# Optimization experiments

Measured on AMD Instinct MI355X. Metric: run time of the kernel, lower is better.

The kernel has to match this reference:

```python
import jax, jax.numpy as jnp
import numpy as np

B, S, D_IN = 2, 2048, 2048
H, KVH, HD = 32, 8, 64
GROUPS = H // KVH
EPS = 1e-6
SCALE = HD ** -0.5


def setup_inputs() -> dict:
    key = jax.random.key(0)
    ks = jax.random.split(key, 6)
    x = jax.random.normal(ks[0], (B, S, D_IN), jnp.float32)
    Wq = jax.random.normal(ks[1], (H * HD, D_IN), jnp.float32) * 0.02
    Wk = jax.random.normal(ks[2], (KVH * HD, D_IN), jnp.float32) * 0.02
    Wv = jax.random.normal(ks[3], (KVH * HD, D_IN), jnp.float32) * 0.02
    Wo = jax.random.normal(ks[4], (D_IN, H * HD), jnp.float32) * 0.02
    w_qnorm = jnp.ones((HD,), jnp.float32)
    w_knorm = jnp.ones((HD,), jnp.float32)
    # Llama-style RoPE tables: [S, HD] with frequencies duplicated across halves
    inv_freq = 1.0 / (10000.0 ** (np.arange(0, HD, 2, dtype=np.float32) / HD))
    ang = np.outer(np.arange(S, dtype=np.float32), inv_freq)  # [S, HD/2]
    emb = np.concatenate([ang, ang], axis=-1)  # [S, HD]
    cos = jnp.asarray(np.cos(emb), jnp.float32)
    sin = jnp.asarray(np.sin(emb), jnp.float32)
    mask = jnp.tril(jnp.ones((S, S), jnp.bool_))  # unused by module (causal hardcoded)
    return dict(x=x, mask=mask, cos=cos, sin=sin, Wq=Wq, Wk=Wk, Wv=Wv, Wo=Wo,
                w_qnorm=w_qnorm, w_knorm=w_knorm)


def _rms_norm(t, w):
    # per-head-dim RMSNorm, eps inside sqrt (torch nn.RMSNorm semantics)
    var = jnp.mean(jnp.square(t), axis=-1, keepdims=True)
    return t * jax.lax.rsqrt(var + EPS) * w


def _rotate_half(t):
    t1, t2 = jnp.split(t, 2, axis=-1)
    return jnp.concatenate([-t2, t1], axis=-1)


def _rope(t, cos, sin):
    # t: [B,H,S,HD]; cos/sin: [S,HD]
    return t * cos[None, None] + _rotate_half(t) * sin[None, None]


def reference(x, mask, cos, sin, Wq, Wk, Wv, Wo, w_qnorm, w_knorm):
    bs, seq, _ = x.shape
    q = (x @ Wq.T).reshape(bs, seq, H, HD).transpose(0, 2, 1, 3)    # [B,H,S,hd]
    k = (x @ Wk.T).reshape(bs, seq, KVH, HD).transpose(0, 2, 1, 3)  # [B,KVH,S,hd]
    v = (x @ Wv.T).reshape(bs, seq, KVH, HD).transpose(0, 2, 1, 3)
    # GQA: repeat_interleave KV over head dim
    k = jnp.repeat(k, GROUPS, axis=1)
    v = jnp.repeat(v, GROUPS, axis=1)
    # fused QK RMSNorm then RoPE
    q = _rope(_rms_norm(q, w_qnorm), cos, sin)
    k = _rope(_rms_norm(k, w_knorm), cos, sin)
    # causal attention
    scores = jnp.einsum('bhqd,bhkd->bhqk', q, k) * SCALE
    causal = jnp.arange(seq)[:, None] >= jnp.arange(seq)[None, :]
    scores = jnp.where(causal, scores, jnp.finfo(scores.dtype).min)
    attn = jax.nn.softmax(scores, axis=-1)
    out = jnp.einsum('bhqk,bhkd->bhqd', attn, v)
    out = out.transpose(0, 2, 1, 3).reshape(bs, seq, H * HD)
    return out @ Wo.T
```

## Files before the change

### kernel.cpp

```cpp
#include <hip/hip_runtime.h>

typedef __bf16 bf16_t;
typedef __bf16 bf16x8 __attribute__((ext_vector_type(8)));
typedef __bf16 bf16x4 __attribute__((ext_vector_type(4)));
typedef float f32x4 __attribute__((ext_vector_type(4)));
typedef unsigned int u32;

#define AS1 __attribute__((address_space(1)))
#define AS3 __attribute__((address_space(3)))

#define ASTR 72

#if __has_builtin(__builtin_amdgcn_exp2f)
#define EXP2(x) __builtin_amdgcn_exp2f(x)
#else
#define EXP2(x) exp2f(x)
#endif

__device__ __forceinline__ void g2l16(const bf16_t* g, bf16_t* l) {
  __builtin_amdgcn_global_load_lds((const AS1 u32*)g, (AS3 u32*)l, 16, 0, 0);
}

__device__ __forceinline__ u32 pkbf(float a, float b) {
  u32 ua = __builtin_bit_cast(u32, a) + 0x8000u;
  u32 ub = __builtin_bit_cast(u32, b) + 0x8000u;
  return (ua >> 16) | (ub & 0xFFFF0000u);
}

__global__ __launch_bounds__(256) void cvt5(
    const float* __restrict__ s0, const float* __restrict__ s1,
    const float* __restrict__ s2, const float* __restrict__ s3,
    const float* __restrict__ s4,
    bf16_t* __restrict__ d0, bf16_t* __restrict__ d1, bf16_t* __restrict__ d2,
    bf16_t* __restrict__ d3, bf16_t* __restrict__ d4)
{
  int blk = blockIdx.x;
  const float* s; bf16_t* d; int off;
  if      (blk <  8192) { s = s0; d = d0; off = blk;         }
  else if (blk < 12288) { s = s1; d = d1; off = blk -  8192; }
  else if (blk < 13312) { s = s2; d = d2; off = blk - 12288; }
  else if (blk < 14336) { s = s3; d = d3; off = blk - 13312; }
  else                  { s = s4; d = d4; off = blk - 14336; }
  size_t i = (size_t)off * 1024 + threadIdx.x * 4;
  float4 v = *(const float4*)&s[i];
  bf16x4 t;
  t[0] = (bf16_t)v.x; t[1] = (bf16_t)v.y; t[2] = (bf16_t)v.z; t[3] = (bf16_t)v.w;
  *(bf16x4*)&d[i] = t;
}

__device__ __forceinline__ void gemm_core(
    const bf16_t* __restrict__ A, const bf16_t* __restrict__ B, int K,
    bf16_t* As0, bf16_t* As1, bf16_t* Bs0, bf16_t* Bs1, f32x4 (&acc)[4][4])
{
  const int tid = threadIdx.x, lane = tid & 63, w = tid >> 6;
  const int col = lane & 15, quad = lane >> 4;
  const int wm = w >> 1, wn = w & 1;
  const int lr = lane >> 2;
  const int lc = (((lane & 3) ^ ((lane >> 3) & 3)) << 3);
  const int sw = ((quad ^ ((col >> 1) & 3)) << 3);
  const bf16_t* ga = A + (size_t)(w * 16 + lr) * K + lc;
  const bf16_t* gb = B + (size_t)(w * 16 + lr) * K + lc;
  const int lo0 = (w * 16) * 32, lo1 = (64 + w * 16) * 32;

  g2l16(ga,                  As0 + lo0);
  g2l16(ga + (size_t)64 * K, As0 + lo1);
  g2l16(gb,                  Bs0 + lo0);
  g2l16(gb + (size_t)64 * K, Bs0 + lo1);

  const int nkb = K >> 5;
  for (int kb = 0; kb < nkb; ++kb) {
    __syncthreads();
    bf16_t* Ac = (kb & 1) ? As1 : As0;
    bf16_t* Bc = (kb & 1) ? Bs1 : Bs0;
    if (kb + 1 < nkb) {
      bf16_t* An = (kb & 1) ? As0 : As1;
      bf16_t* Bn = (kb & 1) ? Bs0 : Bs1;
      const int k2 = (kb + 1) * 32;
      g2l16(ga + k2,                  An + lo0);
      g2l16(ga + k2 + (size_t)64 * K, An + lo1);
      g2l16(gb + k2,                  Bn + lo0);
      g2l16(gb + k2 + (size_t)64 * K, Bn + lo1);
    }

    bf16x8 af[4], bfr[4];
#pragma unroll
    for (int mt = 0; mt < 4; ++mt)
      af[mt] = *(const bf16x8*)&Ac[(wm * 64 + mt * 16 + col) * 32 + sw];
#pragma unroll
    for (int nt = 0; nt < 4; ++nt)
      bfr[nt] = *(const bf16x8*)&Bc[(wn * 64 + nt * 16 + col) * 32 + sw];
#pragma unroll
    for (int mt = 0; mt < 4; ++mt)
#pragma unroll
      for (int nt = 0; nt < 4; ++nt)
        acc[mt][nt] = __builtin_amdgcn_mfma_f32_16x16x32_bf16(af[mt], bfr[nt], acc[mt][nt], 0, 0, 0);
  }
}

__global__ __launch_bounds__(256, 4) void gemm_qkv(
    const bf16_t* __restrict__ xb, const bf16_t* __restrict__ Wqb,
    const bf16_t* __restrict__ Wkb, const bf16_t* __restrict__ Wvb,
    const float* __restrict__ cosT, const float* __restrict__ sinT,
    const float* __restrict__ wq, const float* __restrict__ wk,
    bf16_t* __restrict__ Qn, bf16_t* __restrict__ Kn, bf16_t* __restrict__ Vp)
{
  __shared__ bf16_t As[2][128 * 32], Bs[2][128 * 32];
  const int bn = blockIdx.x, bm = blockIdx.y;
  const bf16_t* B;
  if      (bn < 16) B = Wqb + (size_t)bn * 128 * 2048;
  else if (bn < 20) B = Wkb + (size_t)(bn - 16) * 128 * 2048;
  else              B = Wvb + (size_t)(bn - 20) * 128 * 2048;

  f32x4 acc[4][4] = {};
  gemm_core(xb + (size_t)bm * 128 * 2048, B, 2048, As[0], As[1], Bs[0], Bs[1], acc);

  const int lane = threadIdx.x & 63, w = threadIdx.x >> 6;
  const int col = lane & 15, quad = lane >> 4, wm = w >> 1, wn = w & 1;

  if (bn < 20) {
    const bool isQ = bn < 16;
    const float* wnv = isQ ? wq : wk;
    float w4[4];
#pragma unroll
    for (int nt = 0; nt < 4; ++nt) w4[nt] = wnv[nt * 16 + col];
    bf16_t* dst = isQ ? Qn + ((size_t)(bn * 2 + wn)) * 2048 * 64
                      : Kn + ((size_t)((bn - 16) * 2 + wn)) * 2048 * 64;
    const size_t bstride = isQ ? (size_t)32 * 2048 * 64 : (size_t)8 * 2048 * 64;
    const float qscale = 0.125f * 1.4426950408889634f;

#pragma unroll
    for (int mt = 0; mt < 4; ++mt)
#pragma unroll
      for (int r = 0; r < 4; ++r) {
        int row = bm * 128 + wm * 64 + mt * 16 + quad * 4 + r;
        int b = row >> 11, s = row & 2047;
        float v[4], ss = 0.f;
#pragma unroll
        for (int nt = 0; nt < 4; ++nt) { v[nt] = acc[mt][nt][r]; ss += v[nt] * v[nt]; }
        ss += __shfl_xor(ss, 1, 64);
        ss += __shfl_xor(ss, 2, 64);
        ss += __shfl_xor(ss, 4, 64);
        ss += __shfl_xor(ss, 8, 64);
        float rr = rsqrtf(ss * (1.0f / 64.0f) + 1e-6f);
        float t[4];
#pragma unroll
        for (int nt = 0; nt < 4; ++nt) t[nt] = v[nt] * rr * w4[nt];
        bf16_t* drow = dst + b * bstride + (size_t)s * 64;
#pragma unroll
        for (int nt = 0; nt < 4; ++nt) {
          int hd = nt * 16 + col;
          float rot = (nt < 2) ? -t[nt + 2] : t[nt - 2];
          float ov = t[nt] * cosT[s * 64 + hd] + rot * sinT[s * 64 + hd];
          if (isQ) ov *= qscale;
          drow[hd] = (bf16_t)ov;
        }
      }
  } else {
    const int cb = (bn - 20) * 128;
#pragma unroll
    for (int mt = 0; mt < 4; ++mt)
#pragma unroll
      for (int r = 0; r < 4; ++r) {
        int row = bm * 128 + wm * 64 + mt * 16 + quad * 4 + r;
        bf16_t* crow = Vp + (size_t)row * 512 + cb + wn * 64 + col;
#pragma unroll
        for (int nt = 0; nt < 4; ++nt)
          crow[nt * 16] = (bf16_t)acc[mt][nt][r];
      }
  }
}

__global__ __launch_bounds__(256, 4) void gemm_o(
    const bf16_t* __restrict__ Ao, const bf16_t* __restrict__ Wob,
    float* __restrict__ Cf)
{
  __shared__ bf16_t As[2][128 * 32], Bs[2][128 * 32];
  const int bn = blockIdx.x, bm = blockIdx.y;
  f32x4 acc[4][4] = {};
  gemm_core(Ao + (size_t)bm * 128 * 2048, Wob + (size_t)bn * 128 * 2048, 2048,
            As[0], As[1], Bs[0], Bs[1], acc);

  const int lane = threadIdx.x & 63, w = threadIdx.x >> 6;
  const int col = lane & 15, quad = lane >> 4, wm = w >> 1, wn = w & 1;
#pragma unroll
  for (int mt = 0; mt < 4; ++mt)
#pragma unroll
    for (int r = 0; r < 4; ++r) {
      int row = bm * 128 + wm * 64 + mt * 16 + quad * 4 + r;
      float* crow = Cf + (size_t)row * 2048 + bn * 128 + wn * 64 + col;
#pragma unroll
      for (int nt = 0; nt < 4; ++nt)
        crow[nt * 16] = acc[mt][nt][r];
    }
}

__global__ __launch_bounds__(256) void vtrans(
    const bf16_t* __restrict__ Vp, bf16_t* __restrict__ Vt)
{
  __shared__ bf16_t T[64 * 136];
  const int st = blockIdx.x, kvh = blockIdx.y, b = blockIdx.z;
  const int tid = threadIdx.x;
#pragma unroll
  for (int p = 0; p < 4; ++p) {
    int r = p * 32 + (tid >> 3);
    int c = (tid & 7) * 8;
    bf16x8 v = *(const bf16x8*)&Vp[((size_t)(b * 2048 + st * 128 + r)) * 512 + kvh * 64 + c];
#pragma unroll
    for (int i = 0; i < 8; ++i) T[(c + i) * 136 + r] = v[i];
  }
  __syncthreads();
#pragma unroll
  for (int p = 0; p < 4; ++p) {
    int hd = p * 16 + (tid >> 4);
    int sc = (tid & 15) * 8;
    bf16x8 v = *(const bf16x8*)&T[hd * 136 + sc];
    *(bf16x8*)&Vt[((size_t)((b * 8 + kvh) * 64) + hd) * 2048 + st * 128 + sc] = v;
  }
}

__global__ __launch_bounds__(256, 3) void attn(
    const bf16_t* __restrict__ Qn, const bf16_t* __restrict__ Kn,
    const bf16_t* __restrict__ Vt, bf16_t* __restrict__ Ao)
{
  __shared__ bf16_t KsL[2][64 * 32], KsH[2][64 * 32];
  __shared__ bf16_t VsL[2][64 * 32], VsH[2][64 * 32];
  __shared__ bf16_t Ps[128 * ASTR];

  const int tid = threadIdx.x, lane = tid & 63, w = tid >> 6;
  const int col = lane & 15, quad = lane >> 4;
  const int lr = lane >> 2;
  const int lcs = (((lane & 3) ^ ((lane >> 3) & 3)) << 3);
  const int sw  = ((quad ^ ((col >> 1) & 3)) << 3);
  const int h = blockIdx.x, b = blockIdx.y;
  const int qt = 15 - blockIdx.z;
  const int kvh = h >> 2;

  const bf16_t* Kb = Kn + ((size_t)(b * 8 + kvh)) * 2048 * 64;
  const bf16_t* Vb = Vt + ((size_t)(b * 8 + kvh)) * 64 * 2048;
  const bf16_t* Qb = Qn + (((size_t)(b * 32 + h)) * 2048 + qt * 128) * 64;
  const int lw = w * 512;

  bf16x8 Qf[2][2];
#pragma unroll
  for (int mt = 0; mt < 2; ++mt)
#pragma unroll
    for (int kk = 0; kk < 2; ++kk)
      Qf[mt][kk] = *(const bf16x8*)&Qb[(w * 32 + mt * 16 + col) * 64 + kk * 32 + quad * 8];

  bf16x8 ones;
#pragma unroll
  for (int i = 0; i < 8; ++i) ones[i] = (bf16_t)1.0f;

  f32x4 o[2][4] = {};
  f32x4 lacc[2] = {};

  const int rowmin = qt * 128 + w * 32;
  const int rowmax = rowmin + 31;
  const int jmax = 2 * qt + 1;

  {
    const bf16_t* gk = &Kb[(size_t)(w * 16 + lr) * 64 + lcs];
    const bf16_t* gv = &Vb[(size_t)(w * 16 + lr) * 2048 + lcs];
    g2l16(gk,      &KsL[0][lw]);
    g2l16(gk + 32, &KsH[0][lw]);
    g2l16(gv,      &VsL[0][lw]);
    g2l16(gv + 32, &VsH[0][lw]);
  }

  for (int j = 0; j <= jmax; ++j) {
    __syncthreads();
    if (j < jmax) {
      const int nb = (j + 1) & 1;
      const bf16_t* gk = &Kb[(size_t)((j + 1) * 64 + w * 16 + lr) * 64 + lcs];
      const bf16_t* gv = &Vb[(size_t)(w * 16 + lr) * 2048 + (j + 1) * 64 + lcs];
      g2l16(gk,      &KsL[nb][lw]);
      g2l16(gk + 32, &KsH[nb][lw]);
      g2l16(gv,      &VsL[nb][lw]);
      g2l16(gv + 32, &VsH[nb][lw]);
    }

    if (j * 64 <= rowmax) {
      const int bf = j & 1;
      const bool needmask = (j * 64 + 63 > rowmin);

#pragma unroll
      for (int kt = 0; kt < 4; ++kt) {
        bf16x8 kf0 = *(const bf16x8*)&KsL[bf][(kt * 16 + col) * 32 + sw];
        bf16x8 kf1 = *(const bf16x8*)&KsH[bf][(kt * 16 + col) * 32 + sw];
        f32x4 st0 = {}, st1 = {};
        st0 = __builtin_amdgcn_mfma_f32_16x16x32_bf16(kf0, Qf[0][0], st0, 0, 0, 0);
        st0 = __builtin_amdgcn_mfma_f32_16x16x32_bf16(kf1, Qf[0][1], st0, 0, 0, 0);
        st1 = __builtin_amdgcn_mfma_f32_16x16x32_bf16(kf0, Qf[1][0], st1, 0, 0, 0);
        st1 = __builtin_amdgcn_mfma_f32_16x16x32_bf16(kf1, Qf[1][1], st1, 0, 0, 0);
        const int k0 = j * 64 + kt * 16 + quad * 4;
#pragma unroll
        for (int mt = 0; mt < 2; ++mt) {
          f32x4 st = mt ? st1 : st0;
          float p0 = EXP2(st[0]), p1 = EXP2(st[1]);
          float p2 = EXP2(st[2]), p3 = EXP2(st[3]);
          if (needmask) {
            const int qg = qt * 128 + w * 32 + mt * 16 + col;
            p0 = (k0 + 0 > qg) ? 0.f : p0;
            p1 = (k0 + 1 > qg) ? 0.f : p1;
            p2 = (k0 + 2 > qg) ? 0.f : p2;
            p3 = (k0 + 3 > qg) ? 0.f : p3;
          }
          uint2 pk = { pkbf(p0, p1), pkbf(p2, p3) };
          *(uint2*)&Ps[(w * 32 + mt * 16 + col) * ASTR + kt * 16 + quad * 4] = pk;
        }
      }
      asm volatile("s_waitcnt lgkmcnt(0)" ::: "memory");

#pragma unroll
      for (int kk = 0; kk < 2; ++kk) {
        const bf16_t* Vh = kk ? &VsH[bf][0] : &VsL[bf][0];
        bf16x8 pa0 = *(const bf16x8*)&Ps[(w * 32 + col) * ASTR + kk * 32 + quad * 8];
        bf16x8 pa1 = *(const bf16x8*)&Ps[(w * 32 + 16 + col) * ASTR + kk * 32 + quad * 8];
        lacc[0] = __builtin_amdgcn_mfma_f32_16x16x32_bf16(pa0, ones, lacc[0], 0, 0, 0);
        lacc[1] = __builtin_amdgcn_mfma_f32_16x16x32_bf16(pa1, ones, lacc[1], 0, 0, 0);
#pragma unroll
        for (int nt = 0; nt < 4; ++nt) {
          bf16x8 vf = *(const bf16x8*)&Vh[(nt * 16 + col) * 32 + sw];
          o[0][nt] = __builtin_amdgcn_mfma_f32_16x16x32_bf16(pa0, vf, o[0][nt], 0, 0, 0);
          o[1][nt] = __builtin_amdgcn_mfma_f32_16x16x32_bf16(pa1, vf, o[1][nt], 0, 0, 0);
        }
      }
    }
  }

#pragma unroll
  for (int mt = 0; mt < 2; ++mt)
#pragma unroll
    for (int r = 0; r < 4; ++r) {
      float inv = 1.0f / lacc[mt][r];
      int row = b * 2048 + qt * 128 + w * 32 + mt * 16 + quad * 4 + r;
      bf16_t* orow = &Ao[(size_t)row * 2048 + h * 64 + col];
#pragma unroll
      for (int nt = 0; nt < 4; ++nt)
        orow[nt * 16] = (bf16_t)(o[mt][nt][r] * inv);
    }
}

extern "C" void kernel_launch(void* const* d_in, const int* in_sizes, int n_in,
                              void* d_out, int out_size, void* d_ws, size_t ws_size,
                              hipStream_t stream)
{
  const float* x    = (const float*)d_in[0];
  const float* cosT = (const float*)d_in[2];
  const float* sinT = (const float*)d_in[3];
  const float* Wq   = (const float*)d_in[4];
  const float* Wk   = (const float*)d_in[5];
  const float* Wv   = (const float*)d_in[6];
  const float* Wo   = (const float*)d_in[7];
  const float* wq   = (const float*)d_in[8];
  const float* wk   = (const float*)d_in[9];
  float* out = (float*)d_out;

  char* ws = (char*)d_ws;
  bf16_t* xb  = (bf16_t*)(ws);
  bf16_t* Ao  = (bf16_t*)(ws);
  bf16_t* Wqb = (bf16_t*)(ws + 16777216);
  bf16_t* Vt  = (bf16_t*)(ws + 16777216);
  bf16_t* Wkb = (bf16_t*)(ws + 25165824);
  bf16_t* Wvb = (bf16_t*)(ws + 27262976);
  bf16_t* Wob = (bf16_t*)(ws + 29360128);
  bf16_t* Vp  = (bf16_t*)(ws + 37748736);
  bf16_t* Qn  = (bf16_t*)(ws + 41943040);
  bf16_t* Kn  = (bf16_t*)(ws + 58720256);

  cvt5<<<18432, 256, 0, stream>>>(x, Wq, Wk, Wv, Wo, xb, Wqb, Wkb, Wvb, Wob);
  gemm_qkv<<<dim3(24, 32), 256, 0, stream>>>(xb, Wqb, Wkb, Wvb, cosT, sinT, wq, wk, Qn, Kn, Vp);
  vtrans<<<dim3(16, 8, 2), 256, 0, stream>>>(Vp, Vt);
  attn<<<dim3(32, 2, 16), 256, 0, stream>>>(Qn, Kn, Vt, Ao);
  gemm_o<<<dim3(16, 32), 256, 0, stream>>>(Ao, Wob, out);
}
```

Baseline: 298.6 us.

## Use 256x256 tiles with 4-stage pipelined 8-wave GEMM for QKV projection

Replaces the 128x128, 4-wave, double-buffered QKV GEMM with a 256x256, 8-wave kernel that keeps a 4-deep shared-memory ring fed by direct global-to-LDS loads. MFMA work is interleaved with prefetch, and the kernel raises wave priority around the MFMA blocks. Workgroup indices are remapped into an XCD-aware order to improve L2 reuse. The larger tiles are meant to raise arithmetic intensity and overlap loads with compute. In exchange the grid shrinks to 192 blocks, which may underfill 256 CUs, and the 128 KB of LDS per block limits occupancy.

After: 308.9 us. +3.5%, slower.

```diff
diff --git a/kernel.cpp b/kernel.cpp
--- a/kernel.cpp
+++ b/kernel.cpp
@@ -97,46 +97,121 @@
   }
 }
 
-__global__ __launch_bounds__(256, 4) void gemm_qkv(
+__device__ __forceinline__ void gemm_core8(
+    const bf16_t* __restrict__ A, const bf16_t* __restrict__ B,
+    bf16_t (&As)[4][8192], bf16_t (&Bs)[4][8192], f32x4 (&acc)[8][4])
+{
+  constexpr int NT = 64;
+  const int tid = threadIdx.x, lane = tid & 63, w = tid >> 6;
+  const int col = lane & 15, quad = lane >> 4;
+  const int wm = w >> 2, wn = w & 3;
+  const int lr = lane >> 2;
+  const int lc = (((lane & 3) ^ ((lane >> 3) & 3)) << 3);
+  const int sw = ((quad ^ ((col >> 1) & 3)) << 3);
+  const bf16_t* ga = A + (size_t)(w * 16 + lr) * 2048 + lc;
+  const bf16_t* gb = B + (size_t)(w * 16 + lr) * 2048 + lc;
+  const int lo0 = w * 512, lo1 = 4096 + w * 512;
+
+#pragma unroll
+  for (int tt = 0; tt < 3; ++tt) {
+    g2l16(ga + tt * 32,                      &As[tt][lo0]);
+    g2l16(ga + tt * 32 + (size_t)128 * 2048, &As[tt][lo1]);
+    g2l16(gb + tt * 32,                      &Bs[tt][lo0]);
+    g2l16(gb + tt * 32 + (size_t)128 * 2048, &Bs[tt][lo1]);
+  }
+  asm volatile("s_waitcnt vmcnt(8)" ::: "memory");
+  __builtin_amdgcn_s_barrier();
+
+  for (int t = 0; t < NT; ++t) {
+    const bf16_t* Ac = As[t & 3];
+    const bf16_t* Bc = Bs[t & 3];
+    const int pf = t + 3;
+    bf16x8 bfrg[4], afrg[4];
+
+#pragma unroll
+    for (int nf = 0; nf < 4; ++nf)
+      bfrg[nf] = *(const bf16x8*)&Bc[(wn * 64 + nf * 16 + col) * 32 + sw];
+#pragma unroll
+    for (int mf = 0; mf < 4; ++mf)
+      afrg[mf] = *(const bf16x8*)&Ac[(wm * 128 + mf * 16 + col) * 32 + sw];
+    if (pf < NT) {
+      g2l16(ga + pf * 32,                      &As[pf & 3][lo0]);
+      g2l16(ga + pf * 32 + (size_t)128 * 2048, &As[pf & 3][lo1]);
+    }
+    __builtin_amdgcn_s_barrier();
+    __builtin_amdgcn_s_setprio(1);
+#pragma unroll
+    for (int mf = 0; mf < 4; ++mf)
+#pragma unroll
+      for (int nf = 0; nf < 4; ++nf)
+        acc[mf][nf] = __builtin_amdgcn_mfma_f32_16x16x32_bf16(afrg[mf], bfrg[nf], acc[mf][nf], 0, 0, 0);
+    __builtin_amdgcn_s_setprio(0);
+    __builtin_amdgcn_s_barrier();
+
+#pragma unroll
+    for (int mf = 0; mf < 4; ++mf)
+      afrg[mf] = *(const bf16x8*)&Ac[(wm * 128 + (mf + 4) * 16 + col) * 32 + sw];
+    if (pf < NT) {
+      g2l16(gb + pf * 32,                      &Bs[pf & 3][lo0]);
+      g2l16(gb + pf * 32 + (size_t)128 * 2048, &Bs[pf & 3][lo1]);
+    }
+    __builtin_amdgcn_s_barrier();
+    __builtin_amdgcn_s_setprio(1);
+#pragma unroll
+    for (int mf = 0; mf < 4; ++mf)
+#pragma unroll
+      for (int nf = 0; nf < 4; ++nf)
+        acc[mf + 4][nf] = __builtin_amdgcn_mfma_f32_16x16x32_bf16(afrg[mf], bfrg[nf], acc[mf + 4][nf], 0, 0, 0);
+    __builtin_amdgcn_s_setprio(0);
+    if (t < NT - 3)       asm volatile("s_waitcnt vmcnt(8)" ::: "memory");
+    else if (t == NT - 3) asm volatile("s_waitcnt vmcnt(4)" ::: "memory");
+    else if (t == NT - 2) asm volatile("s_waitcnt vmcnt(0)" ::: "memory");
+    __builtin_amdgcn_s_barrier();
+  }
+}
+
+__global__ __launch_bounds__(512, 2) void gemm_qkv8(
     const bf16_t* __restrict__ xb, const bf16_t* __restrict__ Wqb,
     const bf16_t* __restrict__ Wkb, const bf16_t* __restrict__ Wvb,
     const float* __restrict__ cosT, const float* __restrict__ sinT,
     const float* __restrict__ wq, const float* __restrict__ wk,
     bf16_t* __restrict__ Qn, bf16_t* __restrict__ Kn, bf16_t* __restrict__ Vp)
 {
-  __shared__ bf16_t As[2][128 * 32], Bs[2][128 * 32];
-  const int bn = blockIdx.x, bm = blockIdx.y;
-  const bf16_t* B;
-  if      (bn < 16) B = Wqb + (size_t)bn * 128 * 2048;
-  else if (bn < 20) B = Wkb + (size_t)(bn - 16) * 128 * 2048;
-  else              B = Wvb + (size_t)(bn - 20) * 128 * 2048;
-
-  f32x4 acc[4][4] = {};
-  gemm_core(xb + (size_t)bm * 128 * 2048, B, 2048, As[0], As[1], Bs[0], Bs[1], acc);
+  __shared__ bf16_t As[4][8192], Bs[4][8192];
+  const int bid = blockIdx.x;
+  const int f = (bid & 7) * 24 + (bid >> 3);
+  const int bm = f / 12, bn = f % 12;
+  const bf16_t* Bp;
+  if      (bn <  8) Bp = Wqb + (size_t)bn * 256 * 2048;
+  else if (bn < 10) Bp = Wkb + (size_t)(bn - 8) * 256 * 2048;
+  else              Bp = Wvb + (size_t)(bn - 10) * 256 * 2048;
+
+  f32x4 acc[8][4] = {};
+  gemm_core8(xb + (size_t)bm * 256 * 2048, Bp, As, Bs, acc);
 
   const int lane = threadIdx.x & 63, w = threadIdx.x >> 6;
-  const int col = lane & 15, quad = lane >> 4, wm = w >> 1, wn = w & 1;
-
-  if (bn < 20) {
-    const bool isQ = bn < 16;
+  const int col = lane & 15, quad = lane >> 4, wm = w >> 2, wn = w & 3;
+
+  if (bn < 10) {
+    const bool isQ = bn < 8;
     const float* wnv = isQ ? wq : wk;
     float w4[4];
 #pragma unroll
-    for (int nt = 0; nt < 4; ++nt) w4[nt] = wnv[nt * 16 + col];
-    bf16_t* dst = isQ ? Qn + ((size_t)(bn * 2 + wn)) * 2048 * 64
-                      : Kn + ((size_t)((bn - 16) * 2 + wn)) * 2048 * 64;
+    for (int nf = 0; nf < 4; ++nf) w4[nf] = wnv[nf * 16 + col];
+    const int head = isQ ? bn * 4 + wn : (bn - 8) * 4 + wn;
+    bf16_t* dst = (isQ ? Qn : Kn) + (size_t)head * 2048 * 64;
     const size_t bstride = isQ ? (size_t)32 * 2048 * 64 : (size_t)8 * 2048 * 64;
     const float qscale = 0.125f * 1.4426950408889634f;
 
 #pragma unroll
-    for (int mt = 0; mt < 4; ++mt)
+    for (int mf = 0; mf < 8; ++mf)
 #pragma unroll
       for (int r = 0; r < 4; ++r) {
-        int row = bm * 128 + wm * 64 + mt * 16 + quad * 4 + r;
+        int row = bm * 256 + wm * 128 + mf * 16 + quad * 4 + r;
         int b = row >> 11, s = row & 2047;
         float v[4], ss = 0.f;
 #pragma unroll
-        for (int nt = 0; nt < 4; ++nt) { v[nt] = acc[mt][nt][r]; ss += v[nt] * v[nt]; }
+        for (int nf = 0; nf < 4; ++nf) { v[nf] = acc[mf][nf][r]; ss += v[nf] * v[nf]; }
         ss += __shfl_xor(ss, 1, 64);
         ss += __shfl_xor(ss, 2, 64);
         ss += __shfl_xor(ss, 4, 64);
@@ -144,28 +219,28 @@
         float rr = rsqrtf(ss * (1.0f / 64.0f) + 1e-6f);
         float t[4];
 #pragma unroll
-        for (int nt = 0; nt < 4; ++nt) t[nt] = v[nt] * rr * w4[nt];
+        for (int nf = 0; nf < 4; ++nf) t[nf] = v[nf] * rr * w4[nf];
         bf16_t* drow = dst + b * bstride + (size_t)s * 64;
 #pragma unroll
-        for (int nt = 0; nt < 4; ++nt) {
-          int hd = nt * 16 + col;
-          float rot = (nt < 2) ? -t[nt + 2] : t[nt - 2];
-          float ov = t[nt] * cosT[s * 64 + hd] + rot * sinT[s * 64 + hd];
+        for (int nf = 0; nf < 4; ++nf) {
+          int hd = nf * 16 + col;
+          float rot = (nf < 2) ? -t[nf + 2] : t[nf - 2];
+          float ov = t[nf] * cosT[s * 64 + hd] + rot * sinT[s * 64 + hd];
           if (isQ) ov *= qscale;
           drow[hd] = (bf16_t)ov;
         }
       }
   } else {
-    const int cb = (bn - 20) * 128;
-#pragma unroll
-    for (int mt = 0; mt < 4; ++mt)
+    const int cb = (bn - 10) * 256;
+#pragma unroll
+    for (int mf = 0; mf < 8; ++mf)
 #pragma unroll
       for (int r = 0; r < 4; ++r) {
-        int row = bm * 128 + wm * 64 + mt * 16 + quad * 4 + r;
+        int row = bm * 256 + wm * 128 + mf * 16 + quad * 4 + r;
         bf16_t* crow = Vp + (size_t)row * 512 + cb + wn * 64 + col;
 #pragma unroll
-        for (int nt = 0; nt < 4; ++nt)
-          crow[nt * 16] = (bf16_t)acc[mt][nt][r];
+        for (int nf = 0; nf < 4; ++nf)
+          crow[nf * 16] = (bf16_t)acc[mf][nf][r];
       }
   }
 }
@@ -369,7 +444,7 @@
   bf16_t* Kn  = (bf16_t*)(ws + 58720256);
 
   cvt5<<<18432, 256, 0, stream>>>(x, Wq, Wk, Wv, Wo, xb, Wqb, Wkb, Wvb, Wob);
-  gemm_qkv<<<dim3(24, 32), 256, 0, stream>>>(xb, Wqb, Wkb, Wvb, cosT, sinT, wq, wk, Qn, Kn, Vp);
+  gemm_qkv8<<<192, 512, 0, stream>>>(xb, Wqb, Wkb, Wvb, cosT, sinT, wq, wk, Qn, Kn, Vp);
   vtrans<<<dim3(16, 8, 2), 256, 0, stream>>>(Vp, Vt);
   attn<<<dim3(32, 2, 16), 256, 0, stream>>>(Qn, Kn, Vt, Ao);
   gemm_o<<<dim3(16, 32), 256, 0, stream>>>(Ao, Wob, out);
```

## Triple-buffer GEMM LDS tiles with vmcnt-based waits and single barrier

Applied to the files above, without the earlier changes.

Replaces the double-buffered GEMM mainloop used by the QKV and output projections with a three-stage LDS ring. Loads run two K-steps ahead, and explicit s_waitcnt vmcnt plus a raw s_barrier replace the top-of-loop __syncthreads. The aim is to hide more global-load latency behind the MFMA work. In exchange, LDS per block grows to 48KB, and launch bounds drop from 4 to 3 blocks per CU, which may reduce occupancy.

Result: slower. 314.3 us (+5.2%).

```diff
diff --git a/kernel.cpp b/kernel.cpp
--- a/kernel.cpp
+++ b/kernel.cpp
@@ -48,9 +48,9 @@
   *(bf16x4*)&d[i] = t;
 }
 
-__device__ __forceinline__ void gemm_core(
+__device__ __forceinline__ void gemm_core3(
     const bf16_t* __restrict__ A, const bf16_t* __restrict__ B, int K,
-    bf16_t* As0, bf16_t* As1, bf16_t* Bs0, bf16_t* Bs1, f32x4 (&acc)[4][4])
+    bf16_t (&As)[3][4096], bf16_t (&Bs)[3][4096], f32x4 (&acc)[4][4])
 {
   const int tid = threadIdx.x, lane = tid & 63, w = tid >> 6;
   const int col = lane & 15, quad = lane >> 4;
@@ -62,26 +62,28 @@
   const bf16_t* gb = B + (size_t)(w * 16 + lr) * K + lc;
   const int lo0 = (w * 16) * 32, lo1 = (64 + w * 16) * 32;
 
-  g2l16(ga,                  As0 + lo0);
-  g2l16(ga + (size_t)64 * K, As0 + lo1);
-  g2l16(gb,                  Bs0 + lo0);
-  g2l16(gb + (size_t)64 * K, Bs0 + lo1);
-
   const int nkb = K >> 5;
+
+  g2l16(ga,      &As[0][lo0]); g2l16(ga + (size_t)64 * K,      &As[0][lo1]);
+  g2l16(gb,      &Bs[0][lo0]); g2l16(gb + (size_t)64 * K,      &Bs[0][lo1]);
+  g2l16(ga + 32, &As[1][lo0]); g2l16(ga + 32 + (size_t)64 * K, &As[1][lo1]);
+  g2l16(gb + 32, &Bs[1][lo0]); g2l16(gb + 32 + (size_t)64 * K, &Bs[1][lo1]);
+  asm volatile("s_waitcnt vmcnt(4)" ::: "memory");
+  __builtin_amdgcn_s_barrier();
+
   for (int kb = 0; kb < nkb; ++kb) {
-    __syncthreads();
-    bf16_t* Ac = (kb & 1) ? As1 : As0;
-    bf16_t* Bc = (kb & 1) ? Bs1 : Bs0;
-    if (kb + 1 < nkb) {
-      bf16_t* An = (kb & 1) ? As0 : As1;
-      bf16_t* Bn = (kb & 1) ? Bs0 : Bs1;
-      const int k2 = (kb + 1) * 32;
-      g2l16(ga + k2,                  An + lo0);
-      g2l16(ga + k2 + (size_t)64 * K, An + lo1);
-      g2l16(gb + k2,                  Bn + lo0);
-      g2l16(gb + k2 + (size_t)64 * K, Bn + lo1);
-    }
-
+    if (kb + 2 < nkb) {
+      const int sl = (kb + 2) % 3;
+      const int k2 = (kb + 2) * 32;
+      g2l16(ga + k2,                  &As[sl][lo0]);
+      g2l16(ga + k2 + (size_t)64 * K, &As[sl][lo1]);
+      g2l16(gb + k2,                  &Bs[sl][lo0]);
+      g2l16(gb + k2 + (size_t)64 * K, &Bs[sl][lo1]);
+    }
+
+    const int cu = kb % 3;
+    const bf16_t* Ac = As[cu];
+    const bf16_t* Bc = Bs[cu];
     bf16x8 af[4], bfr[4];
 #pragma unroll
     for (int mt = 0; mt < 4; ++mt)
@@ -94,17 +96,25 @@
 #pragma unroll
       for (int nt = 0; nt < 4; ++nt)
         acc[mt][nt] = __builtin_amdgcn_mfma_f32_16x16x32_bf16(af[mt], bfr[nt], acc[mt][nt], 0, 0, 0);
-  }
-}
-
-__global__ __launch_bounds__(256, 4) void gemm_qkv(
+
+    if (kb + 2 < nkb) {
+      asm volatile("s_waitcnt vmcnt(4)" ::: "memory");
+      __builtin_amdgcn_s_barrier();
+    } else if (kb + 1 < nkb) {
+      asm volatile("s_waitcnt vmcnt(0)" ::: "memory");
+      __builtin_amdgcn_s_barrier();
+    }
+  }
+}
+
+__global__ __launch_bounds__(256, 3) void gemm_qkv(
     const bf16_t* __restrict__ xb, const bf16_t* __restrict__ Wqb,
     const bf16_t* __restrict__ Wkb, const bf16_t* __restrict__ Wvb,
     const float* __restrict__ cosT, const float* __restrict__ sinT,
     const float* __restrict__ wq, const float* __restrict__ wk,
     bf16_t* __restrict__ Qn, bf16_t* __restrict__ Kn, bf16_t* __restrict__ Vp)
 {
-  __shared__ bf16_t As[2][128 * 32], Bs[2][128 * 32];
+  __shared__ bf16_t As[3][4096], Bs[3][4096];
   const int bn = blockIdx.x, bm = blockIdx.y;
   const bf16_t* B;
   if      (bn < 16) B = Wqb + (size_t)bn * 128 * 2048;
@@ -112,7 +122,7 @@
   else              B = Wvb + (size_t)(bn - 20) * 128 * 2048;
 
   f32x4 acc[4][4] = {};
-  gemm_core(xb + (size_t)bm * 128 * 2048, B, 2048, As[0], As[1], Bs[0], Bs[1], acc);
+  gemm_core3(xb + (size_t)bm * 128 * 2048, B, 2048, As, Bs, acc);
 
   const int lane = threadIdx.x & 63, w = threadIdx.x >> 6;
   const int col = lane & 15, quad = lane >> 4, wm = w >> 1, wn = w & 1;
@@ -170,15 +180,15 @@
   }
 }
 
-__global__ __launch_bounds__(256, 4) void gemm_o(
+__global__ __launch_bounds__(256, 3) void gemm_o(
     const bf16_t* __restrict__ Ao, const bf16_t* __restrict__ Wob,
     float* __restrict__ Cf)
 {
-  __shared__ bf16_t As[2][128 * 32], Bs[2][128 * 32];
+  __shared__ bf16_t As[3][4096], Bs[3][4096];
   const int bn = blockIdx.x, bm = blockIdx.y;
   f32x4 acc[4][4] = {};
-  gemm_core(Ao + (size_t)bm * 128 * 2048, Wob + (size_t)bn * 128 * 2048, 2048,
-            As[0], As[1], Bs[0], Bs[1], acc);
+  gemm_core3(Ao + (size_t)bm * 128 * 2048, Wob + (size_t)bn * 128 * 2048, 2048,
+             As, Bs, acc);
 
   const int lane = threadIdx.x & 63, w = threadIdx.x >> 6;
   const int col = lane & 15, quad = lane >> 4, wm = w >> 1, wn = w & 1;
```

## Fuse V transpose into QKV GEMM epilogue and remap blocks per XCD

Applied to the files above, without the earlier changes.

The separate vtrans kernel is removed. The V-projection blocks of gemm_qkv now transpose their accumulators through shared memory and write Vt directly, which drops one launch and a full round trip of V through global memory. Both GEMMs also use a flat grid with an XCD-aware block mapping, so blocks on the same XCD share M-rows for better L2 reuse. The cost is extra syncthreads in the V epilogue and a shared buffer that is reused between GEMM staging and the transpose.

Result: faster. 288.5 us (-3.4%).

```diff
diff --git a/kernel.cpp b/kernel.cpp
--- a/kernel.cpp
+++ b/kernel.cpp
@@ -102,17 +102,19 @@
     const bf16_t* __restrict__ Wkb, const bf16_t* __restrict__ Wvb,
     const float* __restrict__ cosT, const float* __restrict__ sinT,
     const float* __restrict__ wq, const float* __restrict__ wk,
-    bf16_t* __restrict__ Qn, bf16_t* __restrict__ Kn, bf16_t* __restrict__ Vp)
-{
-  __shared__ bf16_t As[2][128 * 32], Bs[2][128 * 32];
-  const int bn = blockIdx.x, bm = blockIdx.y;
+    bf16_t* __restrict__ Qn, bf16_t* __restrict__ Kn, bf16_t* __restrict__ Vt)
+{
+  __shared__ bf16_t S[16384];
+  const int xcd = blockIdx.x & 7, c = blockIdx.x >> 3;
+  const int bm = xcd * 4 + (c & 3), bn = c >> 2;
   const bf16_t* B;
   if      (bn < 16) B = Wqb + (size_t)bn * 128 * 2048;
   else if (bn < 20) B = Wkb + (size_t)(bn - 16) * 128 * 2048;
   else              B = Wvb + (size_t)(bn - 20) * 128 * 2048;
 
   f32x4 acc[4][4] = {};
-  gemm_core(xb + (size_t)bm * 128 * 2048, B, 2048, As[0], As[1], Bs[0], Bs[1], acc);
+  gemm_core(xb + (size_t)bm * 128 * 2048, B, 2048,
+            &S[0], &S[4096], &S[8192], &S[12288], acc);
 
   const int lane = threadIdx.x & 63, w = threadIdx.x >> 6;
   const int col = lane & 15, quad = lane >> 4, wm = w >> 1, wn = w & 1;
@@ -156,17 +158,32 @@
         }
       }
   } else {
-    const int cb = (bn - 20) * 128;
-#pragma unroll
-    for (int mt = 0; mt < 4; ++mt)
-#pragma unroll
-      for (int r = 0; r < 4; ++r) {
-        int row = bm * 128 + wm * 64 + mt * 16 + quad * 4 + r;
-        bf16_t* crow = Vp + (size_t)row * 512 + cb + wn * 64 + col;
-#pragma unroll
-        for (int nt = 0; nt < 4; ++nt)
-          crow[nt * 16] = (bf16_t)acc[mt][nt][r];
-      }
+    const int vb = bn - 20;
+    const int b = bm >> 4, s0 = (bm & 15) * 128;
+    const int tid = threadIdx.x;
+#pragma unroll
+    for (int hh = 0; hh < 2; ++hh) {
+      __syncthreads();
+      if (wn == hh) {
+#pragma unroll
+        for (int mt = 0; mt < 4; ++mt)
+#pragma unroll
+          for (int nt = 0; nt < 4; ++nt)
+#pragma unroll
+            for (int r = 0; r < 4; ++r)
+              S[(nt * 16 + col) * 136 + wm * 64 + mt * 16 + quad * 4 + r] =
+                  (bf16_t)acc[mt][nt][r];
+      }
+      __syncthreads();
+      const int kvh = vb * 2 + hh;
+#pragma unroll
+      for (int p = 0; p < 4; ++p) {
+        int hd = p * 16 + (tid >> 4);
+        int sc = (tid & 15) * 8;
+        bf16x8 v = *(const bf16x8*)&S[hd * 136 + sc];
+        *(bf16x8*)&Vt[((size_t)((b * 8 + kvh) * 64) + hd) * 2048 + s0 + sc] = v;
+      }
+    }
   }
 }
 
@@ -175,7 +192,8 @@
     float* __restrict__ Cf)
 {
   __shared__ bf16_t As[2][128 * 32], Bs[2][128 * 32];
-  const int bn = blockIdx.x, bm = blockIdx.y;
+  const int xcd = blockIdx.x & 7, c = blockIdx.x >> 3;
+  const int bm = xcd * 4 + (c & 3), bn = c >> 2;
   f32x4 acc[4][4] = {};
   gemm_core(Ao + (size_t)bm * 128 * 2048, Wob + (size_t)bn * 128 * 2048, 2048,
             As[0], As[1], Bs[0], Bs[1], acc);
@@ -192,30 +210,6 @@
       for (int nt = 0; nt < 4; ++nt)
         crow[nt * 16] = acc[mt][nt][r];
     }
-}
-
-__global__ __launch_bounds__(256) void vtrans(
-    const bf16_t* __restrict__ Vp, bf16_t* __restrict__ Vt)
-{
-  __shared__ bf16_t T[64 * 136];
-  const int st = blockIdx.x, kvh = blockIdx.y, b = blockIdx.z;
-  const int tid = threadIdx.x;
-#pragma unroll
-  for (int p = 0; p < 4; ++p) {
-    int r = p * 32 + (tid >> 3);
-    int c = (tid & 7) * 8;
-    bf16x8 v = *(const bf16x8*)&Vp[((size_t)(b * 2048 + st * 128 + r)) * 512 + kvh * 64 + c];
-#pragma unroll
-    for (int i = 0; i < 8; ++i) T[(c + i) * 136 + r] = v[i];
-  }
-  __syncthreads();
-#pragma unroll
-  for (int p = 0; p < 4; ++p) {
-    int hd = p * 16 + (tid >> 4);
-    int sc = (tid & 15) * 8;
-    bf16x8 v = *(const bf16x8*)&T[hd * 136 + sc];
-    *(bf16x8*)&Vt[((size_t)((b * 8 + kvh) * 64) + hd) * 2048 + st * 128 + sc] = v;
-  }
 }
 
 __global__ __launch_bounds__(256, 3) void attn(
@@ -360,17 +354,15 @@
   bf16_t* xb  = (bf16_t*)(ws);
   bf16_t* Ao  = (bf16_t*)(ws);
   bf16_t* Wqb = (bf16_t*)(ws + 16777216);
-  bf16_t* Vt  = (bf16_t*)(ws + 16777216);
   bf16_t* Wkb = (bf16_t*)(ws + 25165824);
   bf16_t* Wvb = (bf16_t*)(ws + 27262976);
   bf16_t* Wob = (bf16_t*)(ws + 29360128);
-  bf16_t* Vp  = (bf16_t*)(ws + 37748736);
+  bf16_t* Vt  = (bf16_t*)(ws + 37748736);
   bf16_t* Qn  = (bf16_t*)(ws + 41943040);
   bf16_t* Kn  = (bf16_t*)(ws + 58720256);
 
   cvt5<<<18432, 256, 0, stream>>>(x, Wq, Wk, Wv, Wo, xb, Wqb, Wkb, Wvb, Wob);
-  gemm_qkv<<<dim3(24, 32), 256, 0, stream>>>(xb, Wqb, Wkb, Wvb, cosT, sinT, wq, wk, Qn, Kn, Vp);
-  vtrans<<<dim3(16, 8, 2), 256, 0, stream>>>(Vp, Vt);
+  gemm_qkv<<<768, 256, 0, stream>>>(xb, Wqb, Wkb, Wvb, cosT, sinT, wq, wk, Qn, Kn, Vt);
   attn<<<dim3(32, 2, 16), 256, 0, stream>>>(Qn, Kn, Vt, Ao);
-  gemm_o<<<dim3(16, 32), 256, 0, stream>>>(Ao, Wob, out);
-}
+  gemm_o<<<512, 256, 0, stream>>>(Ao, Wob, out);
+}
```
